# Performance work log

Hardware: AMD Instinct MI355X
Metric: run time of the kernel (lower is better)

Reference implementation:

```python
import jax, jax.numpy as jnp
import numpy as np

N_NODES = 10000
N_EDGES = 160000
MUL = 16            # multiplicity: emb_dim=64, max_l=1 -> irreps 16x0e + 16x1o
EMB = 64
NUM_BASIS = 10
MAX_RADIUS = 4.5
HIDDEN = 64
N_PATHS = 4         # (0e,0e->0e), (0e,1o->1o), (1o,0e->1o), (1o,1o->0e)
W_NUMEL = N_PATHS * MUL * MUL  # 1024


def setup_inputs() -> dict:
    key = jax.random.key(0)
    ks = jax.random.split(key, 6)
    x = jax.random.normal(ks[0], (N_NODES, EMB), jnp.float32)
    src = jax.random.randint(ks[1], (N_EDGES,), 0, N_NODES)
    dst = jax.random.randint(ks[2], (N_EDGES,), 0, N_NODES)
    edge_vec = jax.random.normal(ks[3], (N_EDGES, 3), jnp.float32)
    mlp_w1 = jax.random.normal(ks[4], (NUM_BASIS, HIDDEN), jnp.float32)
    mlp_w2 = jax.random.normal(ks[5], (HIDDEN, W_NUMEL), jnp.float32)
    return {"x": x, "edge_vec": edge_vec, "mlp_w1": mlp_w1,
            "mlp_w2": mlp_w2, "src": src, "dst": dst}


def _sus(t):
    # e3nn smooth bump helper: exp(-1/t) for t>0 else 0
    return jnp.where(t > 0, jnp.exp(-1.0 / jnp.where(t > 0, t, 1.0)), 0.0)


def _radial_embedding(r):
    # soft_one_hot_linspace(basis='smooth_finite', cutoff=True), then *sqrt(num_basis)
    values = jnp.linspace(0.0, MAX_RADIUS, NUM_BASIS + 2)[1:-1]
    step = MAX_RADIUS / (NUM_BASIS + 1)
    diff = (r[:, None] - values) / step                     # [E, NUM_BASIS]
    basis = 1.14136 * jnp.exp(2.0) * _sus(diff + 1.0) * _sus(1.0 - diff)
    return basis * (NUM_BASIS ** 0.5)


def _forward(x, edge_vec, mlp_w1, mlp_w2, src, dst):
    E = edge_vec.shape[0]
    N = x.shape[0]
    r = jnp.linalg.norm(edge_vec, axis=1)                   # [E]
    # spherical harmonics, lmax=1, normalize=True, 'component' norm: Y0=1, Y1=sqrt(3)*n
    y1 = jnp.sqrt(3.0) * edge_vec / r[:, None]              # [E, 3]

    # radial MLP (e3nn FullyConnectedNet: W~N(0,1), x@W/sqrt(fan_in), relu scaled by sqrt(2))
    emb = _radial_embedding(r)                              # [E, 10]
    h = jnp.sqrt(2.0) * jax.nn.relu(emb @ (mlp_w1 / NUM_BASIS ** 0.5))
    w = h @ (mlp_w2 / HIDDEN ** 0.5)                        # [E, 1024]
    w = w.reshape(E, N_PATHS, MUL, MUL)                     # paths in e3nn order A,B,C,D

    xs = x[src]                                             # gather [E, 64]
    x0 = xs[:, :MUL]                                        # [E, 16] 0e scalars
    x1 = xs[:, MUL:].reshape(E, MUL, 3)                     # [E, 16, 3] 1o vectors

    # Fully connected TP normalization ('component', path_norm 'element'):
    # out0 fan = 2*MUL -> alpha 1/(2*MUL); out1 alpha 3/(2*MUL) with w3j 1/sqrt(3)
    c = 1.0 / jnp.sqrt(2.0 * MUL)
    inv_sqrt3 = 1.0 / jnp.sqrt(3.0)
    wA, wB, wC, wD = w[:, 0], w[:, 1], w[:, 2], w[:, 3]
    # 0e outputs: 0e*0e->0e and 1o*1o->0e (dot product, w3j = I/sqrt(3))
    out0 = c * (jnp.einsum('euw,eu->ew', wA, x0)
                + inv_sqrt3 * jnp.einsum('euw,eum,em->ew', wD, x1, y1))
    # 1o outputs: 0e*1o->1o and 1o*0e->1o (w3j = I/sqrt(3), Y0 = 1)
    out1 = c * (jnp.einsum('euw,eu,em->ewm', wB, x0, y1)
                + jnp.einsum('euw,eum->ewm', wC, x1))
    summand = jnp.concatenate([out0, out1.reshape(E, MUL * 3)], axis=1)  # [E, 64]

    out = jax.ops.segment_sum(summand, dst, num_segments=N)             # [N, 64]
    return out * (N / E)


def reference(x, edge_vec, mlp_w1, mlp_w2, src, dst):
    return _forward(x, edge_vec, mlp_w1, mlp_w2, src, dst)
```

## Files before the change

kernel.cpp:

```cpp
#include <hip/hip_runtime.h>
#include <hip/hip_bf16.h>


typedef __attribute__((ext_vector_type(8))) short bf16x8;
typedef __attribute__((ext_vector_type(8))) unsigned short u16x8;
typedef __attribute__((ext_vector_type(4))) float f32x4;

#define NN 10000
#define NE 160000

__device__ __forceinline__ float sus_f(float t) { return t > 0.0f ? __expf(-1.0f / t) : 0.0f; }
__device__ __forceinline__ unsigned int f2bf(float f) {
    unsigned int u = __float_as_uint(f);
    u += 0x7FFFu + ((u >> 16) & 1u);
    return u >> 16;
}
__device__ __forceinline__ float bf2f(unsigned short v) { return __uint_as_float(((unsigned int)v) << 16); }
__device__ __forceinline__ float bflo(unsigned int v) { return __uint_as_float(v << 16); }
__device__ __forceinline__ float bfhi(unsigned int v) { return __uint_as_float(v & 0xFFFF0000u); }
__device__ __forceinline__ float bfe(u16x8 v, int i) { return __uint_as_float(((unsigned int)v[i]) << 16); }

#define GL16(g, l) __builtin_amdgcn_global_load_lds( \
    (const __attribute__((address_space(1))) void*)(g), \
    (__attribute__((address_space(3))) void*)(l), 16, 0, 0)

__device__ __forceinline__ void stageN(const void* g, void* l, int bytes, int tid, int nthr) {
    const char* gc = (const char*)g;
    char* lc = (char*)l;
    const int units = bytes >> 4;
    for (int u = tid; u < units; u += nthr) GL16(gc + ((long)u << 4), lc + (u << 4));
}

__global__ void hist_k(const int* __restrict__ dst, int* __restrict__ hist,
                       const float* __restrict__ w2, char* __restrict__ w2bf) {
    if (blockIdx.x < 625) {
        const int e = blockIdx.x * 256 + threadIdx.x;
        if (e < NE) atomicAdd(&hist[dst[e]], 1);
    } else {
        const int idx = (blockIdx.x - 625) * 256 + threadIdx.x;
        const int j = idx >> 10, R = idx & 1023;
        unsigned int pk[4];
        #pragma unroll
        for (int p = 0; p < 4; ++p) {
            const unsigned int lo = f2bf(w2[(size_t)(8 * j + 2 * p) * 1024 + R]);
            const unsigned int hi = f2bf(w2[(size_t)(8 * j + 2 * p + 1) * 1024 + R]);
            pk[p] = lo | (hi << 16);
        }
        uint4 v; v.x = pk[0]; v.y = pk[1]; v.z = pk[2]; v.w = pk[3];
        *(uint4*)(w2bf + R * 128 + ((j ^ (R & 7)) << 4)) = v;
    }
}

__global__ __launch_bounds__(1024) void scan_k(const int* __restrict__ hist,
                                               int* __restrict__ offsets) {
    __shared__ int hl[NN];
    __shared__ int wsum[16];
    const int tid = threadIdx.x;
    for (int i = tid; i < NN; i += 1024) hl[i] = hist[i];
    __syncthreads();
    const int base = tid * 10;
    int loc[10]; int s = 0;
    #pragma unroll
    for (int i = 0; i < 10; ++i) { loc[i] = s; const int b = base + i; s += (b < NN) ? hl[b] : 0; }
    int v = s;
    const int lane = tid & 63, wv = tid >> 6;
    #pragma unroll
    for (int d = 1; d < 64; d <<= 1) { int t2 = __shfl_up(v, d); if (lane >= d) v += t2; }
    if (lane == 63) wsum[wv] = v;
    __syncthreads();
    if (tid < 64) {
        int w = (tid < 16) ? wsum[tid] : 0;
        #pragma unroll
        for (int d = 1; d < 16; d <<= 1) { int t2 = __shfl_up(w, d); if (tid >= d) w += t2; }
        if (tid < 16) wsum[tid] = w;
    }
    __syncthreads();
    const int wexc = (wv == 0) ? 0 : wsum[wv - 1];
    const int texc = wexc + v - s;
    #pragma unroll
    for (int i = 0; i < 10; ++i) { const int b = base + i; if (b < NN) offsets[b] = texc + loc[i]; }
    if (tid == 1023) offsets[NN] = texc + s;
}

__global__ void scatter_k(const int* __restrict__ dst, const int* __restrict__ offsets,
                          int* __restrict__ cursor, int* __restrict__ perm,
                          int* __restrict__ dsts) {
    const int e = blockIdx.x * 256 + threadIdx.x;
    if (e < NE) {
        const int d = dst[e];
        const int pos = offsets[d] + atomicAdd(&cursor[d], 1);
        perm[pos] = e;
        dsts[pos] = d;
    }
}

__global__ __launch_bounds__(256, 4) void prep_k(
    const float* __restrict__ x, const float* __restrict__ edge_vec,
    const float* __restrict__ w1, const int* __restrict__ src,
    const int* __restrict__ perm,
    char* __restrict__ h_bf, char* __restrict__ X0g, char* __restrict__ Zg,
    char* __restrict__ X1g, float* __restrict__ Y1g)
{
    __shared__ float embl[128][10];
    __shared__ float y1l[128][4];
    __shared__ int srcl[128];
    __shared__ float w1l[640];
    const int tid = threadIdx.x;
    const long e0 = (long)blockIdx.x * 128;

    for (int i = tid; i < 640; i += 256) w1l[i] = w1[i];
    if (tid < 128) {
        const int e = tid;
        const int eid = perm[e0 + e];
        const float vx = edge_vec[eid * 3 + 0];
        const float vy = edge_vec[eid * 3 + 1];
        const float vz = edge_vec[eid * 3 + 2];
        const float r = sqrtf(vx * vx + vy * vy + vz * vz);
        const float sc = 1.7320508075688772f / r;
        y1l[e][0] = vx * sc; y1l[e][1] = vy * sc; y1l[e][2] = vz * sc; y1l[e][3] = 0.f;
        *(float4*)&Y1g[(e0 + e) * 4] = make_float4(vx * sc, vy * sc, vz * sc, 0.f);
        srcl[e] = src[eid];
        const float C0 = 1.14136f * __expf(2.0f) * 3.1622776601683795f;
        #pragma unroll
        for (int i = 0; i < 10; ++i) {
            const float diff = r * (11.0f / 4.5f) - (float)(i + 1);
            embl[e][i] = C0 * sus_f(diff + 1.0f) * sus_f(1.0f - diff);
        }
    }
    __syncthreads();
    for (int idx = tid; idx < 1024; idx += 256) {
        const int e = idx >> 3, j = idx & 7;
        float acc[8];
        #pragma unroll
        for (int jj = 0; jj < 8; ++jj) acc[jj] = 0.0f;
        #pragma unroll
        for (int i = 0; i < 10; ++i) {
            const float ei = embl[e][i];
            #pragma unroll
            for (int jj = 0; jj < 8; ++jj) acc[jj] += ei * w1l[i * 64 + j * 8 + jj];
        }
        unsigned int pk[4];
        #pragma unroll
        for (int p = 0; p < 4; ++p) {
            const unsigned int lo = f2bf(fmaxf(acc[2 * p],     0.0f) * 0.4472135954999579f);
            const unsigned int hi = f2bf(fmaxf(acc[2 * p + 1], 0.0f) * 0.4472135954999579f);
            pk[p] = lo | (hi << 16);
        }
        uint4 v; v.x = pk[0]; v.y = pk[1]; v.z = pk[2]; v.w = pk[3];
        *(uint4*)(h_bf + (e0 + e) * 128 + (j << 4)) = v;
    }
    for (int idx = tid; idx < 1024; idx += 256) {
        const int e = idx >> 3, p = idx & 7;
        const int s = srcl[e];
        const float2 ab = *(const float2*)&x[(size_t)s * 64 + 2 * p];
        *(unsigned int*)(X0g + (e0 + e) * 32 + p * 4) = f2bf(ab.x) | (f2bf(ab.y) << 16);
    }
    for (int idx = tid; idx < 1024; idx += 256) {
        const int e = idx >> 3, p = idx & 7;
        const int s = srcl[e];
        const float* xp = x + (size_t)s * 64 + 16 + 6 * p;
        const float z0 = xp[0] * y1l[e][0] + xp[1] * y1l[e][1] + xp[2] * y1l[e][2];
        const float z1 = xp[3] * y1l[e][0] + xp[4] * y1l[e][1] + xp[5] * y1l[e][2];
        *(unsigned int*)(Zg + (e0 + e) * 32 + p * 4) = f2bf(z0) | (f2bf(z1) << 16);
    }
    for (int idx = tid; idx < 2048; idx += 256) {
        const int e = idx >> 4, u = idx & 15;
        const int s = srcl[e];
        const float* xp = x + (size_t)s * 64 + 16 + 3 * u;
        uint2 v;
        v.x = f2bf(xp[0]) | (f2bf(xp[1]) << 16);
        v.y = f2bf(xp[2]);
        *(uint2*)(X1g + (size_t)blockIdx.x * 16384 + ((u << 7) + e) * 8) = v;
    }
}

#define DSTOFF 22784
#define EBUF 23296

__global__ __launch_bounds__(512, 2) void se3_edge(
    const char* __restrict__ w2bf, const char* __restrict__ h_bf,
    const char* __restrict__ X0g, const char* __restrict__ Zg,
    const char* __restrict__ X1g, const float* __restrict__ Y1g,
    const int* __restrict__ dsts, float* __restrict__ out)
{
    __shared__ __align__(16) char w2lds[65536];
    __shared__ __align__(16) char bufs[2][EBUF];
    __shared__ __align__(16) char summb[12672];
    __shared__ int segst[2][66];
    __shared__ int nseg[2];

    const int tid = threadIdx.x, lane = tid & 63, wv = tid >> 6;
    const int lm = lane & 15, q = lane >> 4, erow = wv << 4;
    const int pair = blockIdx.y;
    const int tb = blockIdx.x;
    const int s0 = (q ^ (lm & 7)) << 4, s1 = s0 ^ 64;
    const float S = 0.17677669529663687f * 0.125f * 0.0625f;

    auto stage_tile = [&](char* nb, long e0) {
        stageN(X0g + e0 * 32, nb, 4096, tid, 512);
        if (pair == 0) {
            stageN(Zg + e0 * 32, nb + 4096, 4096, tid, 512);
        } else {
            stageN(X1g + (e0 >> 7) * 16384, nb + 4096, 16384, tid, 512);
            stageN((const char*)(Y1g + e0 * 4), nb + 20736, 2048, tid, 512);
        }
        stageN((const char*)(dsts + e0), nb + DSTOFF, 512, tid, 512);
    };

    const char* w2p0 = w2lds;
    const char* w2p1 = w2lds + 32768;
    const long e00 = (long)tb * 5 * 128;
    {
        const int pa = pair ? 1 : 0, pb = pair ? 2 : 3;
        stageN(w2bf + pa * 32768, w2lds, 32768, tid, 512);
        stageN(w2bf + pb * 32768, w2lds + 32768, 32768, tid, 512);
        stage_tile(bufs[0], e00);
    }
    __syncthreads();

    const int arow = erow + lm;

    for (int tt = 0; tt < 5; ++tt) {
        char* fb = bufs[tt & 1];
        const long e0 = e00 + (long)tt * 128;
        if (tt < 4) stage_tile(bufs[(tt & 1) ^ 1], e0 + 128);

        const bf16x8 a0 = *(const bf16x8*)(h_bf + (e0 + arow) * 128 + q * 16);
        const bf16x8 a1 = *(const bf16x8*)(h_bf + (e0 + arow) * 128 + 64 + q * 16);

        u16x8 flo[4], fhi[4];
        #pragma unroll
        for (int r = 0; r < 4; ++r) {
            const int el = erow + 4 * q + r;
            flo[r] = *(const u16x8*)(fb + el * 32);
            fhi[r] = *(const u16x8*)(fb + el * 32 + 16);
        }

        float ac0[4] = {0,0,0,0}, ac1[4] = {0,0,0,0}, ac2[4] = {0,0,0,0}, ac3[4] = {0,0,0,0};

        if (pair == 0) {
            u16x8 zlo[4], zhi[4];
            #pragma unroll
            for (int r = 0; r < 4; ++r) {
                const int el = erow + 4 * q + r;
                zlo[r] = *(const u16x8*)(fb + 4096 + el * 32);
                zhi[r] = *(const u16x8*)(fb + 4096 + el * 32 + 16);
            }
            #pragma unroll
            for (int t = 0; t < 16; ++t) {
                const int rowb = (t * 16 + lm) << 7;
                const bf16x8 b00 = *(const bf16x8*)(w2p0 + rowb + s0);
                const bf16x8 b01 = *(const bf16x8*)(w2p0 + rowb + s1);
                const bf16x8 b10 = *(const bf16x8*)(w2p1 + rowb + s0);
                const bf16x8 b11 = *(const bf16x8*)(w2p1 + rowb + s1);
                f32x4 wA = {0.f,0.f,0.f,0.f}, wD = {0.f,0.f,0.f,0.f};
                wA = __builtin_amdgcn_mfma_f32_16x16x32_bf16(a0, b00, wA, 0,0,0);
                wA = __builtin_amdgcn_mfma_f32_16x16x32_bf16(a1, b01, wA, 0,0,0);
                wD = __builtin_amdgcn_mfma_f32_16x16x32_bf16(a0, b10, wD, 0,0,0);
                wD = __builtin_amdgcn_mfma_f32_16x16x32_bf16(a1, b11, wD, 0,0,0);
                #pragma unroll
                for (int r = 0; r < 4; ++r) {
                    ac0[r] += wA[r] * (t < 8 ? bfe(flo[r], t) : bfe(fhi[r], t - 8));
                    ac1[r] += wD[r] * (t < 8 ? bfe(zlo[r], t) : bfe(zhi[r], t - 8));
                }
            }
            float* summ32 = (float*)summb;
            #pragma unroll
            for (int r = 0; r < 4; ++r) {
                const int el = erow + 4 * q + r;
                summ32[lm * 132 + el] = S * (ac0[r] + 0.5773502691896258f * ac1[r]);
            }
        } else {
            #pragma unroll
            for (int t = 0; t < 16; ++t) {
                const int rowb = (t * 16 + lm) << 7;
                const bf16x8 b00 = *(const bf16x8*)(w2p0 + rowb + s0);
                const bf16x8 b01 = *(const bf16x8*)(w2p0 + rowb + s1);
                const bf16x8 b10 = *(const bf16x8*)(w2p1 + rowb + s0);
                const bf16x8 b11 = *(const bf16x8*)(w2p1 + rowb + s1);
                f32x4 wB = {0.f,0.f,0.f,0.f}, wC = {0.f,0.f,0.f,0.f};
                wB = __builtin_amdgcn_mfma_f32_16x16x32_bf16(a0, b00, wB, 0,0,0);
                wB = __builtin_amdgcn_mfma_f32_16x16x32_bf16(a1, b01, wB, 0,0,0);
                wC = __builtin_amdgcn_mfma_f32_16x16x32_bf16(a0, b10, wC, 0,0,0);
                wC = __builtin_amdgcn_mfma_f32_16x16x32_bf16(a1, b11, wC, 0,0,0);
                #pragma unroll
                for (int r = 0; r < 4; ++r) {
                    const int el = erow + 4 * q + r;
                    const uint2 xv = *(const uint2*)(fb + 4096 + ((t << 7) + el) * 8);
                    ac0[r] += wB[r] * (t < 8 ? bfe(flo[r], t) : bfe(fhi[r], t - 8));
                    ac1[r] += wC[r] * bflo(xv.x);
                    ac2[r] += wC[r] * bfhi(xv.x);
                    ac3[r] += wC[r] * bflo(xv.y);
                }
            }
            unsigned short* summ16 = (unsigned short*)summb;
            #pragma unroll
            for (int r = 0; r < 4; ++r) {
                const int el = erow + 4 * q + r;
                const float4 y = *(const float4*)(fb + 20736 + el * 16);
                const float b = S * ac0[r];
                summ16[(3 * lm + 0) * 132 + el] = (unsigned short)f2bf(b * y.x + S * ac1[r]);
                summ16[(3 * lm + 1) * 132 + el] = (unsigned short)f2bf(b * y.y + S * ac2[r]);
                summ16[(3 * lm + 2) * 132 + el] = (unsigned short)f2bf(b * y.z + S * ac3[r]);
            }
        }
        const int* dstl = (const int*)(fb + DSTOFF);
        if (wv < 2) {
            const int base = wv << 6;
            const int d = dstl[base + lane];
            const bool flag = (lane == 0) || (d != dstl[base + lane - 1]);
            const unsigned long long m = __ballot(flag);
            const int sid = (lane == 0) ? 0 : __popcll(m & ((1ull << lane) - 1ull));
            if (flag) segst[wv][sid] = base + lane;
            if (lane == 63) { const int ns = __popcll(m); nseg[wv] = ns; segst[wv][ns] = base + 64; }
        }
        __syncthreads();
        const int nsa = nseg[0], nsb = nseg[1];
        if (pair == 0) {
            const float* sm = (const float*)summb;
            const int total = (nsa + nsb) << 4;
            for (int i = tid; i < total; i += 512) {
                const int sg = i >> 4, c = i & 15;
                const int hh = (sg >= nsa) ? 1 : 0;
                const int sl = hh ? sg - nsa : sg;
                const int eb = segst[hh][sl], ee = segst[hh][sl + 1];
                float s = 0.f;
                for (int e = eb; e < ee; ++e) s += sm[c * 132 + e];
                atomicAdd(&out[(size_t)dstl[eb] * 64 + c], s);
            }
        } else {
            const unsigned short* sm = (const unsigned short*)summb;
            const int total = (nsa + nsb) * 48;
            for (int i = tid; i < total; i += 512) {
                const int sg = i / 48, c = i - sg * 48;
                const int hh = (sg >= nsa) ? 1 : 0;
                const int sl = hh ? sg - nsa : sg;
                const int eb = segst[hh][sl], ee = segst[hh][sl + 1];
                float s = 0.f;
                for (int e = eb; e < ee; ++e) s += bf2f(sm[c * 132 + e]);
                atomicAdd(&out[(size_t)dstl[eb] * 64 + 16 + c], s);
            }
        }
        __syncthreads();
    }
}

#define FBT 64
template<int PATH>
__device__ __forceinline__ void fb_body(
    const float* __restrict__ x, const float* __restrict__ edge_vec,
    const float* __restrict__ w1, const float* __restrict__ w2,
    const int* __restrict__ src, const int* __restrict__ perm,
    const int* __restrict__ dsts, float* __restrict__ out,
    unsigned short (*w2t)[72], float* arena, float (*y1l)[4],
    int* dstl, int* srcl, int* segstart, int* nseg_s)
{
    constexpr int NC    = (PATH == 0 || PATH == 3) ? 16 : 48;
    constexpr int CBASE = (PATH == 0 || PATH == 3) ? 0 : 16;
    const int tid = threadIdx.x;
    float* embl = arena;
    unsigned short* hl = (unsigned short*)(arena + 640);
    float* feats = arena + 2944;
    float* summ  = arena;
    {
        const float* col = w2 + PATH * 256 + tid;
        #pragma unroll
        for (int k = 0; k < 64; k += 2) {
            const unsigned int lo = f2bf(col[(size_t)k * 1024]);
            const unsigned int hi = f2bf(col[(size_t)(k + 1) * 1024]);
            *(unsigned int*)&w2t[tid][k] = lo | (hi << 16);
        }
    }
    const int lane = tid & 63, wv = tid >> 6, lm = lane & 15, q = lane >> 4;
    const int erow = wv * 16;
    const float C0 = 1.14136f * __expf(2.0f) * 3.1622776601683795f;
    const float S  = 0.17677669529663687f * 0.125f * 0.0625f;
    for (int it = 0; it < 2; ++it) {
        const int e0 = (blockIdx.x * 2 + it) * FBT;
        __syncthreads();
        for (int idx = tid; idx < FBT * 10; idx += 256) {
            const int e = idx / 10, i = idx - e * 10;
            const int eid = perm[e0 + e];
            const float vx = edge_vec[eid * 3 + 0], vy = edge_vec[eid * 3 + 1], vz = edge_vec[eid * 3 + 2];
            const float r = sqrtf(vx * vx + vy * vy + vz * vz);
            const float diff = r * (11.0f / 4.5f) - (float)(i + 1);
            embl[e * 10 + i] = C0 * sus_f(diff + 1.0f) * sus_f(1.0f - diff);
            if (i == 0) {
                const float sc = 1.7320508075688772f / r;
                y1l[e][0] = vx * sc; y1l[e][1] = vy * sc; y1l[e][2] = vz * sc;
                dstl[e] = dsts[e0 + e];
                srcl[e] = src[eid];
            }
        }
        __syncthreads();
        for (int idx = tid; idx < FBT * 8; idx += 256) {
            const int e = idx >> 3, j0 = (idx & 7) * 8;
            float acc[8];
            #pragma unroll
            for (int j = 0; j < 8; ++j) acc[j] = 0.0f;
            #pragma unroll
            for (int i = 0; i < 10; ++i) {
                const float ei = embl[e * 10 + i];
                #pragma unroll
                for (int j = 0; j < 8; ++j) acc[j] += ei * w1[i * 64 + j0 + j];
            }
            unsigned int pk[4];
            #pragma unroll
            for (int p = 0; p < 4; ++p) {
                const unsigned int lo = f2bf(fmaxf(acc[2 * p],     0.0f) * 0.4472135954999579f);
                const unsigned int hi = f2bf(fmaxf(acc[2 * p + 1], 0.0f) * 0.4472135954999579f);
                pk[p] = lo | (hi << 16);
            }
            uint4 v; v.x = pk[0]; v.y = pk[1]; v.z = pk[2]; v.w = pk[3];
            *(uint4*)&hl[e * 72 + j0] = v;
        }
        if (PATH == 2) {
            for (int idx = tid; idx < FBT * 48; idx += 256) {
                const int e = idx / 48, c = idx - e * 48;
                feats[e * 48 + c] = x[(size_t)srcl[e] * 64 + 16 + c];
            }
        } else if (PATH == 3) {
            for (int idx = tid; idx < FBT * 16; idx += 256) {
                const int e = idx >> 4, u = idx & 15;
                const float* xs = x + (size_t)srcl[e] * 64 + 16 + u * 3;
                feats[e * 16 + u] = xs[0] * y1l[e][0] + xs[1] * y1l[e][1] + xs[2] * y1l[e][2];
            }
        } else {
            for (int idx = tid; idx < FBT * 16; idx += 256) {
                const int e = idx >> 4, u = idx & 15;
                feats[e * 16 + u] = x[(size_t)srcl[e] * 64 + u];
            }
        }
        __syncthreads();
        const bf16x8 a0 = *(const bf16x8*)&hl[(erow + lm) * 72 + 8 * q];
        const bf16x8 a1 = *(const bf16x8*)&hl[(erow + lm) * 72 + 32 + 8 * q];
        float accO[4] = {0.f,0.f,0.f,0.f}, accC0[4] = {0.f,0.f,0.f,0.f};
        float accC1[4] = {0.f,0.f,0.f,0.f}, accC2[4] = {0.f,0.f,0.f,0.f};
        #pragma unroll 4
        for (int t = 0; t < 16; ++t) {
            const bf16x8 b0 = *(const bf16x8*)&w2t[t * 16 + lm][8 * q];
            const bf16x8 b1 = *(const bf16x8*)&w2t[t * 16 + lm][32 + 8 * q];
            f32x4 wa = {0.f,0.f,0.f,0.f};
            wa = __builtin_amdgcn_mfma_f32_16x16x32_bf16(a0, b0, wa, 0, 0, 0);
            wa = __builtin_amdgcn_mfma_f32_16x16x32_bf16(a1, b1, wa, 0, 0, 0);
            #pragma unroll
            for (int r = 0; r < 4; ++r) {
                const int el = erow + 4 * q + r;
                if (PATH == 2) {
                    accC0[r] += wa[r] * feats[el * 48 + t * 3 + 0];
                    accC1[r] += wa[r] * feats[el * 48 + t * 3 + 1];
                    accC2[r] += wa[r] * feats[el * 48 + t * 3 + 2];
                } else {
                    accO[r] += wa[r] * feats[el * 16 + t];
                }
            }
        }
        __syncthreads();
        #pragma unroll
        for (int r = 0; r < 4; ++r) {
            const int el = erow + 4 * q + r;
            if (PATH == 0) summ[el * 16 + lm] = S * accO[r];
            else if (PATH == 3) summ[el * 16 + lm] = S * 0.5773502691896258f * accO[r];
            else if (PATH == 1) {
                const float tv = S * accO[r];
                summ[el * 48 + lm * 3 + 0] = tv * y1l[el][0];
                summ[el * 48 + lm * 3 + 1] = tv * y1l[el][1];
                summ[el * 48 + lm * 3 + 2] = tv * y1l[el][2];
            } else {
                summ[el * 48 + lm * 3 + 0] = S * accC0[r];
                summ[el * 48 + lm * 3 + 1] = S * accC1[r];
                summ[el * 48 + lm * 3 + 2] = S * accC2[r];
            }
        }
        if (tid < 64) {
            const int d = dstl[tid];
            const bool flag = (tid == 0) || (d != dstl[tid - 1]);
            const unsigned long long m = __ballot(flag);
            const int sid = (tid == 0) ? 0 : __popcll(m & ((1ull << tid) - 1ull));
            if (flag) segstart[sid] = tid;
            if (tid == 63) { const int ns = __popcll(m); *nseg_s = ns; segstart[ns] = 64; }
        }
        __syncthreads();
        const int ns = *nseg_s;
        for (int i = tid; i < ns * NC; i += 256) {
            const int s = i / NC, c = i - s * NC;
            const int eb = segstart[s], ee = segstart[s + 1];
            float sum = 0.0f;
            for (int e = eb; e < ee; ++e) sum += summ[e * NC + c];
            atomicAdd(&out[(size_t)dstl[eb] * 64 + CBASE + c], sum);
        }
    }
}

__global__ __launch_bounds__(256, 2) void fb_edge(
    const float* __restrict__ x, const float* __restrict__ edge_vec,
    const float* __restrict__ w1, const float* __restrict__ w2,
    const int* __restrict__ src, const int* __restrict__ perm,
    const int* __restrict__ dsts, float* __restrict__ out)
{
    __shared__ unsigned short w2t[256][72];
    __shared__ float arena[6016];
    __shared__ float y1l[FBT][4];
    __shared__ int dstl[FBT];
    __shared__ int srcl[FBT];
    __shared__ int segstart[FBT + 1];
    __shared__ int nseg_s;
    switch (blockIdx.y) {
        case 0:  fb_body<0>(x, edge_vec, w1, w2, src, perm, dsts, out, w2t, arena, y1l, dstl, srcl, segstart, &nseg_s); break;
        case 1:  fb_body<1>(x, edge_vec, w1, w2, src, perm, dsts, out, w2t, arena, y1l, dstl, srcl, segstart, &nseg_s); break;
        case 2:  fb_body<2>(x, edge_vec, w1, w2, src, perm, dsts, out, w2t, arena, y1l, dstl, srcl, segstart, &nseg_s); break;
        default: fb_body<3>(x, edge_vec, w1, w2, src, perm, dsts, out, w2t, arena, y1l, dstl, srcl, segstart, &nseg_s); break;
    }
}

extern "C" void kernel_launch(void* const* d_in, const int* in_sizes, int n_in,
                              void* d_out, int out_size, void* d_ws, size_t ws_size,
                              hipStream_t stream) {
    const float* x        = (const float*)d_in[0];
    const float* edge_vec = (const float*)d_in[1];
    const float* w1       = (const float*)d_in[2];
    const float* w2       = (const float*)d_in[3];
    const int*   src      = (const int*)d_in[4];
    const int*   dst      = (const int*)d_in[5];
    float* out = (float*)d_out;

    char* ws = (char*)d_ws;
    size_t off = 0;
    auto alloc = [&](size_t n) -> char* {
        off = (off + 255) & ~(size_t)255;
        char* p = ws + off; off += n; return p;
    };
    int* hist    = (int*)alloc(40000);
    int* cursor  = (int*)alloc(40000);
    int* offsets = (int*)alloc(40004);
    int* perm    = (int*)alloc(640000);
    int* dsts    = (int*)alloc(640000);
    char* w2bf   = alloc(131072);
    char* h_bf   = alloc((size_t)NE * 128);
    char* X0g    = alloc((size_t)NE * 32);
    char* Zg     = alloc((size_t)NE * 32);
    char* X1g    = alloc((size_t)NE * 128);
    float* Y1g   = (float*)alloc((size_t)NE * 16);
    const bool big = (off <= ws_size);

    hipMemsetAsync(d_out, 0, (size_t)out_size * sizeof(float), stream);
    hipMemsetAsync(d_ws, 0, 81408, stream);

    if (big) {
        hipLaunchKernelGGL(hist_k, dim3(657), dim3(256), 0, stream, dst, hist, w2, w2bf);
        hipLaunchKernelGGL(scan_k, dim3(1), dim3(1024), 0, stream, hist, offsets);
        hipLaunchKernelGGL(scatter_k, dim3(625), dim3(256), 0, stream, dst, offsets, cursor, perm, dsts);
        hipLaunchKernelGGL(prep_k, dim3(1250), dim3(256), 0, stream,
                           x, edge_vec, w1, src, perm, h_bf, X0g, Zg, X1g, Y1g);
        hipLaunchKernelGGL(se3_edge, dim3(250, 2), dim3(512), 0, stream,
                           w2bf, h_bf, X0g, Zg, X1g, Y1g, dsts, out);
    } else {
        hipLaunchKernelGGL(hist_k, dim3(625), dim3(256), 0, stream, dst, hist, w2, w2bf);
        hipLaunchKernelGGL(scan_k, dim3(1), dim3(1024), 0, stream, hist, offsets);
        hipLaunchKernelGGL(scatter_k, dim3(625), dim3(256), 0, stream, dst, offsets, cursor, perm, dsts);
        hipLaunchKernelGGL(fb_edge, dim3(1250, 4), dim3(256), 0, stream,
                           x, edge_vec, w1, w2, src, perm, dsts, out);
    }
}
```

Measured before the change: 127.5 us.

## Fuse per-edge prep into the edge kernel and drop intermediate buffers

Removes the separate prep kernel and its global intermediates (radial hidden h, bf16 x0/z/x1 gathers, y1). Each tile of the edge kernel now computes the radial embedding, the first MLP layer, the spherical harmonics and the bf16 gathers of x in shared memory, and scatter now also writes a sorted src array. The aim is to save the global write and re-read of the intermediates and one kernel launch. In exchange, both pair blocks redo the prep work, the double-buffered global-to-LDS staging of the next tile is gone, and the trailing loop barrier is removed.

```diff
diff --git a/kernel.cpp b/kernel.cpp
--- a/kernel.cpp
+++ b/kernel.cpp
@@ -82,188 +82,165 @@
     if (tid == 1023) offsets[NN] = texc + s;
 }
 
-__global__ void scatter_k(const int* __restrict__ dst, const int* __restrict__ offsets,
+__global__ void scatter_k(const int* __restrict__ dst, const int* __restrict__ src,
+                          const int* __restrict__ offsets,
                           int* __restrict__ cursor, int* __restrict__ perm,
-                          int* __restrict__ dsts) {
+                          int* __restrict__ dsts, int* __restrict__ srcg) {
     const int e = blockIdx.x * 256 + threadIdx.x;
     if (e < NE) {
         const int d = dst[e];
         const int pos = offsets[d] + atomicAdd(&cursor[d], 1);
         perm[pos] = e;
         dsts[pos] = d;
-    }
-}
-
-__global__ __launch_bounds__(256, 4) void prep_k(
-    const float* __restrict__ x, const float* __restrict__ edge_vec,
-    const float* __restrict__ w1, const int* __restrict__ src,
-    const int* __restrict__ perm,
-    char* __restrict__ h_bf, char* __restrict__ X0g, char* __restrict__ Zg,
-    char* __restrict__ X1g, float* __restrict__ Y1g)
-{
-    __shared__ float embl[128][10];
-    __shared__ float y1l[128][4];
-    __shared__ int srcl[128];
-    __shared__ float w1l[640];
-    const int tid = threadIdx.x;
-    const long e0 = (long)blockIdx.x * 128;
-
-    for (int i = tid; i < 640; i += 256) w1l[i] = w1[i];
-    if (tid < 128) {
-        const int e = tid;
-        const int eid = perm[e0 + e];
-        const float vx = edge_vec[eid * 3 + 0];
-        const float vy = edge_vec[eid * 3 + 1];
-        const float vz = edge_vec[eid * 3 + 2];
-        const float r = sqrtf(vx * vx + vy * vy + vz * vz);
-        const float sc = 1.7320508075688772f / r;
-        y1l[e][0] = vx * sc; y1l[e][1] = vy * sc; y1l[e][2] = vz * sc; y1l[e][3] = 0.f;
-        *(float4*)&Y1g[(e0 + e) * 4] = make_float4(vx * sc, vy * sc, vz * sc, 0.f);
-        srcl[e] = src[eid];
-        const float C0 = 1.14136f * __expf(2.0f) * 3.1622776601683795f;
-        #pragma unroll
-        for (int i = 0; i < 10; ++i) {
-            const float diff = r * (11.0f / 4.5f) - (float)(i + 1);
-            embl[e][i] = C0 * sus_f(diff + 1.0f) * sus_f(1.0f - diff);
-        }
-    }
-    __syncthreads();
-    for (int idx = tid; idx < 1024; idx += 256) {
-        const int e = idx >> 3, j = idx & 7;
-        float acc[8];
-        #pragma unroll
-        for (int jj = 0; jj < 8; ++jj) acc[jj] = 0.0f;
-        #pragma unroll
-        for (int i = 0; i < 10; ++i) {
-            const float ei = embl[e][i];
-            #pragma unroll
-            for (int jj = 0; jj < 8; ++jj) acc[jj] += ei * w1l[i * 64 + j * 8 + jj];
-        }
-        unsigned int pk[4];
-        #pragma unroll
-        for (int p = 0; p < 4; ++p) {
-            const unsigned int lo = f2bf(fmaxf(acc[2 * p],     0.0f) * 0.4472135954999579f);
-            const unsigned int hi = f2bf(fmaxf(acc[2 * p + 1], 0.0f) * 0.4472135954999579f);
-            pk[p] = lo | (hi << 16);
-        }
-        uint4 v; v.x = pk[0]; v.y = pk[1]; v.z = pk[2]; v.w = pk[3];
-        *(uint4*)(h_bf + (e0 + e) * 128 + (j << 4)) = v;
-    }
-    for (int idx = tid; idx < 1024; idx += 256) {
-        const int e = idx >> 3, p = idx & 7;
-        const int s = srcl[e];
-        const float2 ab = *(const float2*)&x[(size_t)s * 64 + 2 * p];
-        *(unsigned int*)(X0g + (e0 + e) * 32 + p * 4) = f2bf(ab.x) | (f2bf(ab.y) << 16);
-    }
-    for (int idx = tid; idx < 1024; idx += 256) {
-        const int e = idx >> 3, p = idx & 7;
-        const int s = srcl[e];
-        const float* xp = x + (size_t)s * 64 + 16 + 6 * p;
-        const float z0 = xp[0] * y1l[e][0] + xp[1] * y1l[e][1] + xp[2] * y1l[e][2];
-        const float z1 = xp[3] * y1l[e][0] + xp[4] * y1l[e][1] + xp[5] * y1l[e][2];
-        *(unsigned int*)(Zg + (e0 + e) * 32 + p * 4) = f2bf(z0) | (f2bf(z1) << 16);
-    }
-    for (int idx = tid; idx < 2048; idx += 256) {
-        const int e = idx >> 4, u = idx & 15;
-        const int s = srcl[e];
-        const float* xp = x + (size_t)s * 64 + 16 + 3 * u;
-        uint2 v;
-        v.x = f2bf(xp[0]) | (f2bf(xp[1]) << 16);
-        v.y = f2bf(xp[2]);
-        *(uint2*)(X1g + (size_t)blockIdx.x * 16384 + ((u << 7) + e) * 8) = v;
-    }
-}
-
-#define DSTOFF 22784
-#define EBUF 23296
+        if (srcg) srcg[pos] = src[e];
+    }
+}
 
 __global__ __launch_bounds__(512, 2) void se3_edge(
-    const char* __restrict__ w2bf, const char* __restrict__ h_bf,
-    const char* __restrict__ X0g, const char* __restrict__ Zg,
-    const char* __restrict__ X1g, const float* __restrict__ Y1g,
+    const char* __restrict__ w2bf, const float* __restrict__ x,
+    const float* __restrict__ edge_vec, const float* __restrict__ w1,
+    const int* __restrict__ perm, const int* __restrict__ srcg,
     const int* __restrict__ dsts, float* __restrict__ out)
 {
     __shared__ __align__(16) char w2lds[65536];
-    __shared__ __align__(16) char bufs[2][EBUF];
+    __shared__ __align__(16) char x0l[4096];
+    __shared__ __align__(16) char x1Tl[16384];
+    __shared__ float y1l[128][4];
+    __shared__ float embl[128][10];
+    __shared__ __align__(16) float w1l[640];
+    __shared__ __align__(16) int meta[1920];
     __shared__ __align__(16) char summb[12672];
     __shared__ int segst[2][66];
     __shared__ int nseg[2];
 
     const int tid = threadIdx.x, lane = tid & 63, wv = tid >> 6;
     const int lm = lane & 15, q = lane >> 4, erow = wv << 4;
+    const int tb = blockIdx.x;
     const int pair = blockIdx.y;
-    const int tb = blockIdx.x;
     const int s0 = (q ^ (lm & 7)) << 4, s1 = s0 ^ 64;
+    const int sel = tid >> 2, sa = tid & 3;
     const float S = 0.17677669529663687f * 0.125f * 0.0625f;
-
-    auto stage_tile = [&](char* nb, long e0) {
-        stageN(X0g + e0 * 32, nb, 4096, tid, 512);
-        if (pair == 0) {
-            stageN(Zg + e0 * 32, nb + 4096, 4096, tid, 512);
-        } else {
-            stageN(X1g + (e0 >> 7) * 16384, nb + 4096, 16384, tid, 512);
-            stageN((const char*)(Y1g + e0 * 4), nb + 20736, 2048, tid, 512);
-        }
-        stageN((const char*)(dsts + e0), nb + DSTOFF, 512, tid, 512);
-    };
-
-    const char* w2p0 = w2lds;
-    const char* w2p1 = w2lds + 32768;
-    const long e00 = (long)tb * 5 * 128;
+    const float C0 = 1.14136f * __expf(2.0f) * 3.1622776601683795f;
+    const long e00 = (long)tb * 640;
+
     {
         const int pa = pair ? 1 : 0, pb = pair ? 2 : 3;
         stageN(w2bf + pa * 32768, w2lds, 32768, tid, 512);
         stageN(w2bf + pb * 32768, w2lds + 32768, 32768, tid, 512);
-        stage_tile(bufs[0], e00);
+        stageN((const char*)(perm + e00), meta,        2560, tid, 512);
+        stageN((const char*)(srcg + e00), meta + 640,  2560, tid, 512);
+        stageN((const char*)(dsts + e00), meta + 1280, 2560, tid, 512);
+        stageN((const char*)w1, w1l, 2560, tid, 512);
     }
     __syncthreads();
 
+    const char* w2p0 = w2lds;
+    const char* w2p1 = w2lds + 32768;
     const int arow = erow + lm;
 
     for (int tt = 0; tt < 5; ++tt) {
-        char* fb = bufs[tt & 1];
-        const long e0 = e00 + (long)tt * 128;
-        if (tt < 4) stage_tile(bufs[(tt & 1) ^ 1], e0 + 128);
-
-        const bf16x8 a0 = *(const bf16x8*)(h_bf + (e0 + arow) * 128 + q * 16);
-        const bf16x8 a1 = *(const bf16x8*)(h_bf + (e0 + arow) * 128 + 64 + q * 16);
+        const int eb = tt << 7;
+        {
+            const int eid = meta[eb + sel];
+            const int s   = meta[640 + eb + sel];
+            const float vx = edge_vec[eid * 3 + 0];
+            const float vy = edge_vec[eid * 3 + 1];
+            const float vz = edge_vec[eid * 3 + 2];
+            const float r = sqrtf(vx * vx + vy * vy + vz * vz);
+            if (sa == 0) {
+                const float sc = 1.7320508075688772f / r;
+                *(float4*)&y1l[sel][0] = make_float4(vx * sc, vy * sc, vz * sc, 0.f);
+            }
+            #pragma unroll
+            for (int i = sa; i < 10; i += 4) {
+                const float diff = r * (11.0f / 4.5f) - (float)(i + 1);
+                embl[sel][i] = C0 * sus_f(diff + 1.0f) * sus_f(1.0f - diff);
+            }
+            const float4 v0 = *(const float4*)&x[(size_t)s * 64 + 4 * sa];
+            uint2 p0;
+            p0.x = f2bf(v0.x) | (f2bf(v0.y) << 16);
+            p0.y = f2bf(v0.z) | (f2bf(v0.w) << 16);
+            *(uint2*)(x0l + sel * 32 + sa * 8) = p0;
+            const float* xp = &x[(size_t)s * 64 + 16 + 12 * sa];
+            const float4 q0 = *(const float4*)xp;
+            const float4 q1 = *(const float4*)(xp + 4);
+            const float4 q2 = *(const float4*)(xp + 8);
+            const float f[12] = { q0.x, q0.y, q0.z, q0.w, q1.x, q1.y,
+                                  q1.z, q1.w, q2.x, q2.y, q2.z, q2.w };
+            #pragma unroll
+            for (int k = 0; k < 4; ++k) {
+                uint2 v;
+                v.x = f2bf(f[3 * k]) | (f2bf(f[3 * k + 1]) << 16);
+                v.y = f2bf(f[3 * k + 2]);
+                *(uint2*)(x1Tl + (((4 * sa + k) << 7) + sel) * 8) = v;
+            }
+        }
+        __syncthreads();
+
+        float ha[8], hb[8];
+        #pragma unroll
+        for (int jj = 0; jj < 8; ++jj) { ha[jj] = 0.f; hb[jj] = 0.f; }
+        #pragma unroll
+        for (int i = 0; i < 10; ++i) {
+            const float ei = embl[arow][i];
+            const float4 wa0 = *(const float4*)&w1l[i * 64 + 8 * q];
+            const float4 wa1 = *(const float4*)&w1l[i * 64 + 8 * q + 4];
+            const float4 wb0 = *(const float4*)&w1l[i * 64 + 32 + 8 * q];
+            const float4 wb1 = *(const float4*)&w1l[i * 64 + 36 + 8 * q];
+            ha[0] += ei * wa0.x; ha[1] += ei * wa0.y; ha[2] += ei * wa0.z; ha[3] += ei * wa0.w;
+            ha[4] += ei * wa1.x; ha[5] += ei * wa1.y; ha[6] += ei * wa1.z; ha[7] += ei * wa1.w;
+            hb[0] += ei * wb0.x; hb[1] += ei * wb0.y; hb[2] += ei * wb0.z; hb[3] += ei * wb0.w;
+            hb[4] += ei * wb1.x; hb[5] += ei * wb1.y; hb[6] += ei * wb1.z; hb[7] += ei * wb1.w;
+        }
+        bf16x8 a0, a1;
+        #pragma unroll
+        for (int jj = 0; jj < 8; ++jj) {
+            a0[jj] = (short)f2bf(fmaxf(ha[jj], 0.0f) * 0.4472135954999579f);
+            a1[jj] = (short)f2bf(fmaxf(hb[jj], 0.0f) * 0.4472135954999579f);
+        }
 
         u16x8 flo[4], fhi[4];
+        float4 ye[4];
         #pragma unroll
         for (int r = 0; r < 4; ++r) {
             const int el = erow + 4 * q + r;
-            flo[r] = *(const u16x8*)(fb + el * 32);
-            fhi[r] = *(const u16x8*)(fb + el * 32 + 16);
+            flo[r] = *(const u16x8*)(x0l + el * 32);
+            fhi[r] = *(const u16x8*)(x0l + el * 32 + 16);
+            ye[r]  = *(const float4*)&y1l[el][0];
         }
 
         float ac0[4] = {0,0,0,0}, ac1[4] = {0,0,0,0}, ac2[4] = {0,0,0,0}, ac3[4] = {0,0,0,0};
-
-        if (pair == 0) {
-            u16x8 zlo[4], zhi[4];
+        #pragma unroll
+        for (int t = 0; t < 16; ++t) {
+            const int rowb = (t * 16 + lm) << 7;
+            const bf16x8 b00 = *(const bf16x8*)(w2p0 + rowb + s0);
+            const bf16x8 b01 = *(const bf16x8*)(w2p0 + rowb + s1);
+            const bf16x8 b10 = *(const bf16x8*)(w2p1 + rowb + s0);
+            const bf16x8 b11 = *(const bf16x8*)(w2p1 + rowb + s1);
+            f32x4 wP = {0.f,0.f,0.f,0.f}, wQ = {0.f,0.f,0.f,0.f};
+            wP = __builtin_amdgcn_mfma_f32_16x16x32_bf16(a0, b00, wP, 0,0,0);
+            wP = __builtin_amdgcn_mfma_f32_16x16x32_bf16(a1, b01, wP, 0,0,0);
+            wQ = __builtin_amdgcn_mfma_f32_16x16x32_bf16(a0, b10, wQ, 0,0,0);
+            wQ = __builtin_amdgcn_mfma_f32_16x16x32_bf16(a1, b11, wQ, 0,0,0);
             #pragma unroll
             for (int r = 0; r < 4; ++r) {
                 const int el = erow + 4 * q + r;
-                zlo[r] = *(const u16x8*)(fb + 4096 + el * 32);
-                zhi[r] = *(const u16x8*)(fb + 4096 + el * 32 + 16);
-            }
-            #pragma unroll
-            for (int t = 0; t < 16; ++t) {
-                const int rowb = (t * 16 + lm) << 7;
-                const bf16x8 b00 = *(const bf16x8*)(w2p0 + rowb + s0);
-                const bf16x8 b01 = *(const bf16x8*)(w2p0 + rowb + s1);
-                const bf16x8 b10 = *(const bf16x8*)(w2p1 + rowb + s0);
-                const bf16x8 b11 = *(const bf16x8*)(w2p1 + rowb + s1);
-                f32x4 wA = {0.f,0.f,0.f,0.f}, wD = {0.f,0.f,0.f,0.f};
-                wA = __builtin_amdgcn_mfma_f32_16x16x32_bf16(a0, b00, wA, 0,0,0);
-                wA = __builtin_amdgcn_mfma_f32_16x16x32_bf16(a1, b01, wA, 0,0,0);
-                wD = __builtin_amdgcn_mfma_f32_16x16x32_bf16(a0, b10, wD, 0,0,0);
-                wD = __builtin_amdgcn_mfma_f32_16x16x32_bf16(a1, b11, wD, 0,0,0);
-                #pragma unroll
-                for (int r = 0; r < 4; ++r) {
-                    ac0[r] += wA[r] * (t < 8 ? bfe(flo[r], t) : bfe(fhi[r], t - 8));
-                    ac1[r] += wD[r] * (t < 8 ? bfe(zlo[r], t) : bfe(zhi[r], t - 8));
+                const uint2 xv = *(const uint2*)(x1Tl + (((t << 7) + el)) * 8);
+                const float x0v = (t < 8) ? bfe(flo[r], t) : bfe(fhi[r], t - 8);
+                ac0[r] += wP[r] * x0v;
+                if (pair == 0) {
+                    const float zv = bflo(xv.x) * ye[r].x + bfhi(xv.x) * ye[r].y
+                                   + bflo(xv.y) * ye[r].z;
+                    ac1[r] += wQ[r] * zv;
+                } else {
+                    ac1[r] += wQ[r] * bflo(xv.x);
+                    ac2[r] += wQ[r] * bfhi(xv.x);
+                    ac3[r] += wQ[r] * bflo(xv.y);
                 }
             }
+        }
+
+        if (pair == 0) {
             float* summ32 = (float*)summb;
             #pragma unroll
             for (int r = 0; r < 4; ++r) {
@@ -271,40 +248,17 @@
                 summ32[lm * 132 + el] = S * (ac0[r] + 0.5773502691896258f * ac1[r]);
             }
         } else {
-            #pragma unroll
-            for (int t = 0; t < 16; ++t) {
-                const int rowb = (t * 16 + lm) << 7;
-                const bf16x8 b00 = *(const bf16x8*)(w2p0 + rowb + s0);
-                const bf16x8 b01 = *(const bf16x8*)(w2p0 + rowb + s1);
-                const bf16x8 b10 = *(const bf16x8*)(w2p1 + rowb + s0);
-                const bf16x8 b11 = *(const bf16x8*)(w2p1 + rowb + s1);
-                f32x4 wB = {0.f,0.f,0.f,0.f}, wC = {0.f,0.f,0.f,0.f};
-                wB = __builtin_amdgcn_mfma_f32_16x16x32_bf16(a0, b00, wB, 0,0,0);
-                wB = __builtin_amdgcn_mfma_f32_16x16x32_bf16(a1, b01, wB, 0,0,0);
-                wC = __builtin_amdgcn_mfma_f32_16x16x32_bf16(a0, b10, wC, 0,0,0);
-                wC = __builtin_amdgcn_mfma_f32_16x16x32_bf16(a1, b11, wC, 0,0,0);
-                #pragma unroll
-                for (int r = 0; r < 4; ++r) {
-                    const int el = erow + 4 * q + r;
-                    const uint2 xv = *(const uint2*)(fb + 4096 + ((t << 7) + el) * 8);
-                    ac0[r] += wB[r] * (t < 8 ? bfe(flo[r], t) : bfe(fhi[r], t - 8));
-                    ac1[r] += wC[r] * bflo(xv.x);
-                    ac2[r] += wC[r] * bfhi(xv.x);
-                    ac3[r] += wC[r] * bflo(xv.y);
-                }
-            }
             unsigned short* summ16 = (unsigned short*)summb;
             #pragma unroll
             for (int r = 0; r < 4; ++r) {
                 const int el = erow + 4 * q + r;
-                const float4 y = *(const float4*)(fb + 20736 + el * 16);
                 const float b = S * ac0[r];
-                summ16[(3 * lm + 0) * 132 + el] = (unsigned short)f2bf(b * y.x + S * ac1[r]);
-                summ16[(3 * lm + 1) * 132 + el] = (unsigned short)f2bf(b * y.y + S * ac2[r]);
-                summ16[(3 * lm + 2) * 132 + el] = (unsigned short)f2bf(b * y.z + S * ac3[r]);
-            }
-        }
-        const int* dstl = (const int*)(fb + DSTOFF);
+                summ16[(3 * lm + 0) * 132 + el] = (unsigned short)f2bf(b * ye[r].x + S * ac1[r]);
+                summ16[(3 * lm + 1) * 132 + el] = (unsigned short)f2bf(b * ye[r].y + S * ac2[r]);
+                summ16[(3 * lm + 2) * 132 + el] = (unsigned short)f2bf(b * ye[r].z + S * ac3[r]);
+            }
+        }
+        const int* dstl = meta + 1280 + eb;
         if (wv < 2) {
             const int base = wv << 6;
             const int d = dstl[base + lane];
@@ -315,6 +269,7 @@
             if (lane == 63) { const int ns = __popcll(m); nseg[wv] = ns; segst[wv][ns] = base + 64; }
         }
         __syncthreads();
+
         const int nsa = nseg[0], nsb = nseg[1];
         if (pair == 0) {
             const float* sm = (const float*)summb;
@@ -323,10 +278,10 @@
                 const int sg = i >> 4, c = i & 15;
                 const int hh = (sg >= nsa) ? 1 : 0;
                 const int sl = hh ? sg - nsa : sg;
-                const int eb = segst[hh][sl], ee = segst[hh][sl + 1];
+                const int ebg = segst[hh][sl], ee = segst[hh][sl + 1];
                 float s = 0.f;
-                for (int e = eb; e < ee; ++e) s += sm[c * 132 + e];
-                atomicAdd(&out[(size_t)dstl[eb] * 64 + c], s);
+                for (int e = ebg; e < ee; ++e) s += sm[c * 132 + e];
+                atomicAdd(&out[(size_t)dstl[ebg] * 64 + c], s);
             }
         } else {
             const unsigned short* sm = (const unsigned short*)summb;
@@ -335,13 +290,12 @@
                 const int sg = i / 48, c = i - sg * 48;
                 const int hh = (sg >= nsa) ? 1 : 0;
                 const int sl = hh ? sg - nsa : sg;
-                const int eb = segst[hh][sl], ee = segst[hh][sl + 1];
+                const int ebg = segst[hh][sl], ee = segst[hh][sl + 1];
                 float s = 0.f;
-                for (int e = eb; e < ee; ++e) s += bf2f(sm[c * 132 + e]);
-                atomicAdd(&out[(size_t)dstl[eb] * 64 + 16 + c], s);
-            }
-        }
-        __syncthreads();
+                for (int e = ebg; e < ee; ++e) s += bf2f(sm[c * 132 + e]);
+                atomicAdd(&out[(size_t)dstl[ebg] * 64 + 16 + c], s);
+            }
+        }
     }
 }
 
@@ -535,12 +489,8 @@
     int* offsets = (int*)alloc(40004);
     int* perm    = (int*)alloc(640000);
     int* dsts    = (int*)alloc(640000);
+    int* srcg    = (int*)alloc(640000);
     char* w2bf   = alloc(131072);
-    char* h_bf   = alloc((size_t)NE * 128);
-    char* X0g    = alloc((size_t)NE * 32);
-    char* Zg     = alloc((size_t)NE * 32);
-    char* X1g    = alloc((size_t)NE * 128);
-    float* Y1g   = (float*)alloc((size_t)NE * 16);
     const bool big = (off <= ws_size);
 
     hipMemsetAsync(d_out, 0, (size_t)out_size * sizeof(float), stream);
@@ -549,15 +499,15 @@
     if (big) {
         hipLaunchKernelGGL(hist_k, dim3(657), dim3(256), 0, stream, dst, hist, w2, w2bf);
         hipLaunchKernelGGL(scan_k, dim3(1), dim3(1024), 0, stream, hist, offsets);
-        hipLaunchKernelGGL(scatter_k, dim3(625), dim3(256), 0, stream, dst, offsets, cursor, perm, dsts);
-        hipLaunchKernelGGL(prep_k, dim3(1250), dim3(256), 0, stream,
-                           x, edge_vec, w1, src, perm, h_bf, X0g, Zg, X1g, Y1g);
+        hipLaunchKernelGGL(scatter_k, dim3(625), dim3(256), 0, stream,
+                           dst, src, offsets, cursor, perm, dsts, srcg);
         hipLaunchKernelGGL(se3_edge, dim3(250, 2), dim3(512), 0, stream,
-                           w2bf, h_bf, X0g, Zg, X1g, Y1g, dsts, out);
+                           w2bf, x, edge_vec, w1, perm, srcg, dsts, out);
     } else {
         hipLaunchKernelGGL(hist_k, dim3(625), dim3(256), 0, stream, dst, hist, w2, w2bf);
         hipLaunchKernelGGL(scan_k, dim3(1), dim3(1024), 0, stream, hist, offsets);
-        hipLaunchKernelGGL(scatter_k, dim3(625), dim3(256), 0, stream, dst, offsets, cursor, perm, dsts);
+        hipLaunchKernelGGL(scatter_k, dim3(625), dim3(256), 0, stream,
+                           dst, src, offsets, cursor, perm, dsts, (int*)nullptr);
         hipLaunchKernelGGL(fb_edge, dim3(1250, 4), dim3(256), 0, stream,
                            x, edge_vec, w1, w2, src, perm, dsts, out);
     }
```

Measured after the change: 153.5 us. 1.2x slower.
